# Kernel optimization log

Hardware: AMD Instinct MI355X
Metric: run time of the kernel (lower is better)

## Reference

```python
import jax, jax.numpy as jnp
import numpy as np

HIDDEN = 128
HEADS = 8
HEAD_DIM = HIDDEN // HEADS


def setup_inputs() -> dict:
    key = jax.random.key(0)
    ks = jax.random.split(key, 10)
    B, V = 2, 768
    s = 1.0 / np.sqrt(HIDDEN)
    return {
        "x": jax.random.normal(ks[0], (B, V, HIDDEN), dtype=jnp.float32),
        "edge_gate": jax.random.uniform(ks[1], (B, V, V, HIDDEN), dtype=jnp.float32),
        "Wq": jax.random.normal(ks[2], (HIDDEN, HIDDEN), dtype=jnp.float32) * s,
        "bq": jnp.zeros((HIDDEN,), dtype=jnp.float32),
        "Wk": jax.random.normal(ks[3], (HIDDEN, HIDDEN), dtype=jnp.float32) * s,
        "bk": jnp.zeros((HIDDEN,), dtype=jnp.float32),
        "Wv": jax.random.normal(ks[4], (HIDDEN, HIDDEN), dtype=jnp.float32) * s,
        "bv": jnp.zeros((HIDDEN,), dtype=jnp.float32),
        "Wo": jax.random.normal(ks[5], (HIDDEN, HIDDEN), dtype=jnp.float32) * s,
        "bo": jnp.zeros((HIDDEN,), dtype=jnp.float32),
    }


def reference(x, edge_gate, Wq, bq, Wk, bk, Wv, bv, Wo, bo):
    B, V, H = x.shape
    nh, hd = HEADS, HEAD_DIM
    # torch Linear: y = x @ W.T + b
    q = (x @ Wq.T + bq).reshape(B, V, nh, hd).transpose(0, 2, 1, 3)  # (B,nh,V,hd)
    k = (x @ Wk.T + bk).reshape(B, V, nh, hd).transpose(0, 2, 1, 3)
    v = (x @ Wv.T + bv).reshape(B, V, nh, hd).transpose(0, 2, 1, 3)
    scores = jnp.einsum("bhqd,bhkd->bhqk", q, k) / jnp.sqrt(jnp.float32(hd))
    edge_mask = jnp.mean(edge_gate, axis=-1)[:, None]  # (B,1,V,V)
    weights = jax.nn.softmax(scores * edge_mask, axis=-1)
    attended = jnp.einsum("bhqk,bhkd->bhqd", weights, v)
    attended = attended.transpose(0, 2, 1, 3).reshape(B, V, H)
    return attended @ Wo.T + bo
```

## Files before the change

### kernel.cpp

```cpp
#include <hip/hip_runtime.h>
#include <math.h>

#define BB 2
#define VV 768
#define HID 128
#define NH 8
#define HD 16

__global__ __launch_bounds__(256) void edge_mean_kernel(
    const float* __restrict__ eg, float* __restrict__ mask) {
    const int lane = threadIdx.x & 63;
    const long long NPAIR = (long long)BB * VV * VV / 2;
    long long w  = (long long)blockIdx.x * (blockDim.x >> 6) + (threadIdx.x >> 6);
    long long nw = (long long)gridDim.x * (blockDim.x >> 6);
    for (long long p = w; p < NPAIR; p += nw) {
        float4 v = ((const float4*)eg)[p * 64 + lane];
        float s = v.x + v.y + v.z + v.w;
        s += __shfl_xor(s, 1);
        s += __shfl_xor(s, 2);
        s += __shfl_xor(s, 4);
        s += __shfl_xor(s, 8);
        s += __shfl_xor(s, 16);
        if ((lane & 31) == 0)
            mask[p * 2 + (lane >> 5)] = s * (1.0f / 128.0f);
    }
}

__global__ __launch_bounds__(128) void qkv_kernel(
    const float* __restrict__ x,
    const float* __restrict__ Wq, const float* __restrict__ bq,
    const float* __restrict__ Wk, const float* __restrict__ bk,
    const float* __restrict__ Wv, const float* __restrict__ bv,
    float* __restrict__ qh, float* __restrict__ kh, float* __restrict__ vh) {
    const int row = blockIdx.x;
    const int c   = threadIdx.x;
    __shared__ float xs[HID];
    xs[c] = x[row * HID + c];
    __syncthreads();
    const float4* xs4 = (const float4*)xs;
    const float4* wq4 = (const float4*)(Wq + c * HID);
    const float4* wk4 = (const float4*)(Wk + c * HID);
    const float4* wv4 = (const float4*)(Wv + c * HID);
    float aq = 0.f, ak = 0.f, av = 0.f;
#pragma unroll
    for (int k4 = 0; k4 < HID / 4; ++k4) {
        float4 xv = xs4[k4];
        float4 a = wq4[k4];
        aq += xv.x * a.x + xv.y * a.y + xv.z * a.z + xv.w * a.w;
        float4 bqv = wk4[k4];
        ak += xv.x * bqv.x + xv.y * bqv.y + xv.z * bqv.z + xv.w * bqv.w;
        float4 cv = wv4[k4];
        av += xv.x * cv.x + xv.y * cv.y + xv.z * cv.z + xv.w * cv.w;
    }
    const int b = row / VV, vi = row - b * VV;
    const int idx = ((b * NH + (c >> 4)) * VV + vi) * HD + (c & 15);
    qh[idx] = aq + bq[c];
    kh[idx] = ak + bk[c];
    vh[idx] = av + bv[c];
}

__global__ __launch_bounds__(256) void attn_kernel(
    const float* __restrict__ qh, const float* __restrict__ kh,
    const float* __restrict__ vh, const float* __restrict__ mask,
    float* __restrict__ att) {
    __shared__ float sc[4][VV];
    const int wid  = threadIdx.x >> 6;
    const int lane = threadIdx.x & 63;
    const int gw   = blockIdx.x * 4 + wid;
    const int qi   = gw % VV;
    const int bh   = gw / VV;
    const int b    = bh >> 3, h = bh & 7;

    const float4* qp = (const float4*)(qh + (size_t)(bh * VV + qi) * HD);
    const float4 q0 = qp[0], q1 = qp[1], q2 = qp[2], q3 = qp[3];

    const float* mrow = mask + (size_t)(b * VV + qi) * VV;
    const float* kbase = kh + (size_t)bh * VV * HD;
    const float* vbase = vh + (size_t)bh * VV * HD;

    float m = -INFINITY;
#pragma unroll
    for (int t = 0; t < VV / 64; ++t) {
        const int j = lane + 64 * t;
        const float4* kp = (const float4*)(kbase + j * HD);
        float4 k0 = kp[0], k1 = kp[1], k2 = kp[2], k3 = kp[3];
        float dot = q0.x * k0.x + q0.y * k0.y + q0.z * k0.z + q0.w * k0.w
                  + q1.x * k1.x + q1.y * k1.y + q1.z * k1.z + q1.w * k1.w
                  + q2.x * k2.x + q2.y * k2.y + q2.z * k2.z + q2.w * k2.w
                  + q3.x * k3.x + q3.y * k3.y + q3.z * k3.z + q3.w * k3.w;
        float s = dot * 0.25f * mrow[j];
        sc[wid][j] = s;
        m = fmaxf(m, s);
    }
#pragma unroll
    for (int off = 1; off < 64; off <<= 1) m = fmaxf(m, __shfl_xor(m, off));

    float sum = 0.f;
    float acc[HD];
#pragma unroll
    for (int d = 0; d < HD; ++d) acc[d] = 0.f;
#pragma unroll
    for (int t = 0; t < VV / 64; ++t) {
        const int j = lane + 64 * t;
        float e = __expf(sc[wid][j] - m);
        sum += e;
        const float4* vp = (const float4*)(vbase + j * HD);
        float4 v0 = vp[0], v1 = vp[1], v2 = vp[2], v3 = vp[3];
        acc[0]  += e * v0.x; acc[1]  += e * v0.y; acc[2]  += e * v0.z; acc[3]  += e * v0.w;
        acc[4]  += e * v1.x; acc[5]  += e * v1.y; acc[6]  += e * v1.z; acc[7]  += e * v1.w;
        acc[8]  += e * v2.x; acc[9]  += e * v2.y; acc[10] += e * v2.z; acc[11] += e * v2.w;
        acc[12] += e * v3.x; acc[13] += e * v3.y; acc[14] += e * v3.z; acc[15] += e * v3.w;
    }
#pragma unroll
    for (int off = 1; off < 64; off <<= 1) {
        sum += __shfl_xor(sum, off);
#pragma unroll
        for (int d = 0; d < HD; ++d) acc[d] += __shfl_xor(acc[d], off);
    }

    const float inv = 1.0f / sum;
    float outv = 0.f;
#pragma unroll
    for (int d = 0; d < HD; ++d)
        if (lane == d) outv = acc[d];
    if (lane < HD)
        att[(size_t)(b * VV + qi) * HID + h * HD + lane] = outv * inv;
}

__global__ __launch_bounds__(128) void outproj_kernel(
    const float* __restrict__ att, const float* __restrict__ Wo,
    const float* __restrict__ bo, float* __restrict__ out) {
    const int row = blockIdx.x;
    const int c   = threadIdx.x;
    __shared__ float xs[HID];
    xs[c] = att[row * HID + c];
    __syncthreads();
    const float4* xs4 = (const float4*)xs;
    const float4* wo4 = (const float4*)(Wo + c * HID);
    float a = 0.f;
#pragma unroll
    for (int k4 = 0; k4 < HID / 4; ++k4) {
        float4 xv = xs4[k4];
        float4 wv = wo4[k4];
        a += xv.x * wv.x + xv.y * wv.y + xv.z * wv.z + xv.w * wv.w;
    }
    out[row * HID + c] = a + bo[c];
}

extern "C" void kernel_launch(void* const* d_in, const int* in_sizes, int n_in,
                              void* d_out, int out_size, void* d_ws, size_t ws_size,
                              hipStream_t stream) {
    const float* x  = (const float*)d_in[0];
    const float* eg = (const float*)d_in[1];
    const float* Wq = (const float*)d_in[2];
    const float* bq = (const float*)d_in[3];
    const float* Wk = (const float*)d_in[4];
    const float* bk = (const float*)d_in[5];
    const float* Wv = (const float*)d_in[6];
    const float* bv = (const float*)d_in[7];
    const float* Wo = (const float*)d_in[8];
    const float* bo = (const float*)d_in[9];
    float* out = (float*)d_out;

    float* ws   = (float*)d_ws;
    float* mask = ws;
    float* qh   = mask + (size_t)BB * VV * VV;
    float* kh   = qh + (size_t)BB * VV * HID;
    float* vh   = kh + (size_t)BB * VV * HID;
    float* att  = vh + (size_t)BB * VV * HID;

    hipLaunchKernelGGL(edge_mean_kernel, dim3(2048), dim3(256), 0, stream, eg, mask);
    hipLaunchKernelGGL(qkv_kernel, dim3(BB * VV), dim3(128), 0, stream,
                       x, Wq, bq, Wk, bk, Wv, bv, qh, kh, vh);
    hipLaunchKernelGGL(attn_kernel, dim3(BB * NH * VV / 4), dim3(256), 0, stream,
                       qh, kh, vh, mask, att);
    hipLaunchKernelGGL(outproj_kernel, dim3(BB * VV), dim3(128), 0, stream,
                       att, Wo, bo, out);
}
```

Before: 240.1 us.

## Fuse QKV projection with edge-mean and use transpose-style attention reduction

Merges the edge-gate mean kernel and the QKV projection into one launch, with block ranges split between the two tasks, so the small QKV work runs alongside the bandwidth-bound edge reduction. The edge loop becomes a fixed trip count with unrolling. The attention output reduction changes from a full butterfly over 16 accumulators to a recursive-halving exchange, which cuts the number of cross-lane shuffles. The lane-to-dimension mapping is now bit-reversed, which adds some index complexity.

Result: no change. 243.5 us (+1.4%).

```diff
diff --git a/kernel.cpp b/kernel.cpp
--- a/kernel.cpp
+++ b/kernel.cpp
@@ -7,56 +7,64 @@
 #define NH 8
 #define HD 16
 
-__global__ __launch_bounds__(256) void edge_mean_kernel(
-    const float* __restrict__ eg, float* __restrict__ mask) {
-    const int lane = threadIdx.x & 63;
-    const long long NPAIR = (long long)BB * VV * VV / 2;
-    long long w  = (long long)blockIdx.x * (blockDim.x >> 6) + (threadIdx.x >> 6);
-    long long nw = (long long)gridDim.x * (blockDim.x >> 6);
-    for (long long p = w; p < NPAIR; p += nw) {
-        float4 v = ((const float4*)eg)[p * 64 + lane];
-        float s = v.x + v.y + v.z + v.w;
-        s += __shfl_xor(s, 1);
-        s += __shfl_xor(s, 2);
-        s += __shfl_xor(s, 4);
-        s += __shfl_xor(s, 8);
-        s += __shfl_xor(s, 16);
-        if ((lane & 31) == 0)
-            mask[p * 2 + (lane >> 5)] = s * (1.0f / 128.0f);
-    }
-}
-
-__global__ __launch_bounds__(128) void qkv_kernel(
-    const float* __restrict__ x,
+#define QKV_BLOCKS 768
+#define EDGE_BLOCKS 2048
+#define EDGE_WAVES (EDGE_BLOCKS * 4)
+#define NPAIR (BB * VV * VV / 2)
+#define EDGE_ITERS (NPAIR / EDGE_WAVES)
+
+__global__ __launch_bounds__(256) void fused_qkv_edgemean(
+    const float* __restrict__ x, const float* __restrict__ eg,
     const float* __restrict__ Wq, const float* __restrict__ bq,
     const float* __restrict__ Wk, const float* __restrict__ bk,
     const float* __restrict__ Wv, const float* __restrict__ bv,
-    float* __restrict__ qh, float* __restrict__ kh, float* __restrict__ vh) {
-    const int row = blockIdx.x;
-    const int c   = threadIdx.x;
-    __shared__ float xs[HID];
-    xs[c] = x[row * HID + c];
-    __syncthreads();
-    const float4* xs4 = (const float4*)xs;
-    const float4* wq4 = (const float4*)(Wq + c * HID);
-    const float4* wk4 = (const float4*)(Wk + c * HID);
-    const float4* wv4 = (const float4*)(Wv + c * HID);
-    float aq = 0.f, ak = 0.f, av = 0.f;
-#pragma unroll
-    for (int k4 = 0; k4 < HID / 4; ++k4) {
-        float4 xv = xs4[k4];
-        float4 a = wq4[k4];
-        aq += xv.x * a.x + xv.y * a.y + xv.z * a.z + xv.w * a.w;
-        float4 bqv = wk4[k4];
-        ak += xv.x * bqv.x + xv.y * bqv.y + xv.z * bqv.z + xv.w * bqv.w;
-        float4 cv = wv4[k4];
-        av += xv.x * cv.x + xv.y * cv.y + xv.z * cv.z + xv.w * cv.w;
-    }
-    const int b = row / VV, vi = row - b * VV;
-    const int idx = ((b * NH + (c >> 4)) * VV + vi) * HD + (c & 15);
-    qh[idx] = aq + bq[c];
-    kh[idx] = ak + bk[c];
-    vh[idx] = av + bv[c];
+    float* __restrict__ qh, float* __restrict__ kh, float* __restrict__ vh,
+    float* __restrict__ mask) {
+    __shared__ float xs[2][HID];
+    if (blockIdx.x < QKV_BLOCKS) {
+        const int half = threadIdx.x >> 7;
+        const int c    = threadIdx.x & 127;
+        const int row  = blockIdx.x * 2 + half;
+        xs[half][c] = x[row * HID + c];
+        __syncthreads();
+        const float4* xs4 = (const float4*)xs[half];
+        const float4* wq4 = (const float4*)(Wq + c * HID);
+        const float4* wk4 = (const float4*)(Wk + c * HID);
+        const float4* wv4 = (const float4*)(Wv + c * HID);
+        float aq = 0.f, ak = 0.f, av = 0.f;
+#pragma unroll
+        for (int k4 = 0; k4 < HID / 4; ++k4) {
+            float4 xv = xs4[k4];
+            float4 a = wq4[k4];
+            aq += xv.x * a.x + xv.y * a.y + xv.z * a.z + xv.w * a.w;
+            float4 bv2 = wk4[k4];
+            ak += xv.x * bv2.x + xv.y * bv2.y + xv.z * bv2.z + xv.w * bv2.w;
+            float4 cv = wv4[k4];
+            av += xv.x * cv.x + xv.y * cv.y + xv.z * cv.z + xv.w * cv.w;
+        }
+        const int b = row / VV, vi = row - b * VV;
+        const int idx = ((b * NH + (c >> 4)) * VV + vi) * HD + (c & 15);
+        qh[idx] = aq + bq[c];
+        kh[idx] = ak + bk[c];
+        vh[idx] = av + bv[c];
+    } else {
+        const int lane = threadIdx.x & 63;
+        const int w = (blockIdx.x - QKV_BLOCKS) * 4 + (threadIdx.x >> 6);
+        const float4* eg4 = (const float4*)eg;
+#pragma unroll 4
+        for (int it = 0; it < EDGE_ITERS; ++it) {
+            const int p = w + it * EDGE_WAVES;
+            float4 v = eg4[(size_t)p * 64 + lane];
+            float s = v.x + v.y + v.z + v.w;
+            s += __shfl_xor(s, 1);
+            s += __shfl_xor(s, 2);
+            s += __shfl_xor(s, 4);
+            s += __shfl_xor(s, 8);
+            s += __shfl_xor(s, 16);
+            if ((lane & 31) == 0)
+                mask[p * 2 + (lane >> 5)] = s * (1.0f / 128.0f);
+        }
+    }
 }
 
 __global__ __launch_bounds__(256) void attn_kernel(
@@ -74,7 +82,7 @@
     const float4* qp = (const float4*)(qh + (size_t)(bh * VV + qi) * HD);
     const float4 q0 = qp[0], q1 = qp[1], q2 = qp[2], q3 = qp[3];
 
-    const float* mrow = mask + (size_t)(b * VV + qi) * VV;
+    const float* mrow  = mask + (size_t)(b * VV + qi) * VV;
     const float* kbase = kh + (size_t)bh * VV * HD;
     const float* vbase = vh + (size_t)bh * VV * HD;
 
@@ -112,19 +120,38 @@
         acc[12] += e * v3.x; acc[13] += e * v3.y; acc[14] += e * v3.z; acc[15] += e * v3.w;
     }
 #pragma unroll
-    for (int off = 1; off < 64; off <<= 1) {
-        sum += __shfl_xor(sum, off);
-#pragma unroll
-        for (int d = 0; d < HD; ++d) acc[d] += __shfl_xor(acc[d], off);
-    }
+    for (int off = 1; off < 64; off <<= 1) sum += __shfl_xor(sum, off);
+
+#pragma unroll
+    for (int i = 0; i < 8; ++i) {
+        float send = (lane & 1) ? acc[i] : acc[i + 8];
+        float r = __shfl_xor(send, 1);
+        acc[i] = ((lane & 1) ? acc[i + 8] : acc[i]) + r;
+    }
+#pragma unroll
+    for (int i = 0; i < 4; ++i) {
+        float send = (lane & 2) ? acc[i] : acc[i + 4];
+        float r = __shfl_xor(send, 2);
+        acc[i] = ((lane & 2) ? acc[i + 4] : acc[i]) + r;
+    }
+#pragma unroll
+    for (int i = 0; i < 2; ++i) {
+        float send = (lane & 4) ? acc[i] : acc[i + 2];
+        float r = __shfl_xor(send, 4);
+        acc[i] = ((lane & 4) ? acc[i + 2] : acc[i]) + r;
+    }
+    {
+        float send = (lane & 8) ? acc[0] : acc[1];
+        float r = __shfl_xor(send, 8);
+        acc[0] = ((lane & 8) ? acc[1] : acc[0]) + r;
+    }
+    acc[0] += __shfl_xor(acc[0], 16);
+    acc[0] += __shfl_xor(acc[0], 32);
 
     const float inv = 1.0f / sum;
-    float outv = 0.f;
-#pragma unroll
-    for (int d = 0; d < HD; ++d)
-        if (lane == d) outv = acc[d];
+    const int d = ((lane & 1) << 3) | ((lane & 2) << 1) | ((lane & 4) >> 1) | ((lane & 8) >> 3);
     if (lane < HD)
-        att[(size_t)(b * VV + qi) * HID + h * HD + lane] = outv * inv;
+        att[(size_t)(b * VV + qi) * HID + h * HD + d] = acc[0] * inv;
 }
 
 __global__ __launch_bounds__(128) void outproj_kernel(
@@ -169,9 +196,8 @@
     float* vh   = kh + (size_t)BB * VV * HID;
     float* att  = vh + (size_t)BB * VV * HID;
 
-    hipLaunchKernelGGL(edge_mean_kernel, dim3(2048), dim3(256), 0, stream, eg, mask);
-    hipLaunchKernelGGL(qkv_kernel, dim3(BB * VV), dim3(128), 0, stream,
-                       x, Wq, bq, Wk, bk, Wv, bv, qh, kh, vh);
+    hipLaunchKernelGGL(fused_qkv_edgemean, dim3(QKV_BLOCKS + EDGE_BLOCKS), dim3(256), 0, stream,
+                       x, eg, Wq, bq, Wk, bk, Wv, bv, qh, kh, vh, mask);
     hipLaunchKernelGGL(attn_kernel, dim3(BB * NH * VV / 4), dim3(256), 0, stream,
                        qh, kh, vh, mask, att);
     hipLaunchKernelGGL(outproj_kernel, dim3(BB * VV), dim3(128), 0, stream,
```
